# Kernel tuning notes

Measured on AMD Instinct MI355X. Metric: run time of the kernel, lower is better.

The kernel has to match this reference:

```python
import jax, jax.numpy as jnp
import numpy as np

P_EPS = 1e-6            # nn.PairwiseDistance default eps
ALPHA = 0.25
STD_TARGET = 1.0
NUM_COMMUNITIES = 512   # C = number of unique community ids
BIG = 1e30              # masking value for hard-negative min


def setup_inputs() -> dict:
    key = jax.random.key(0)
    k1, k2, k3 = jax.random.split(key, 3)
    B, N, D, C = 1, 100000, 128, NUM_COMMUNITIES
    node_features = jax.random.normal(k1, (B, N, D), dtype=jnp.float32)
    # row 0: a permutation of node indices; row 1: community of that node.
    perm = jax.random.permutation(k2, N).astype(jnp.int32)
    comm_per_node = jnp.concatenate([
        jnp.arange(C, dtype=jnp.int32),  # guarantee every community appears
        jax.random.randint(k3, (N - C,), 0, C, dtype=jnp.int32),
    ])
    community_belong_list = jnp.stack([perm, comm_per_node[perm]])  # [2, N]
    return {"node_features": node_features, "community_belong_list": community_belong_list}


def reference(node_features, community_belong_list):
    B, N, D = node_features.shape
    C = NUM_COMMUNITIES
    dt = node_features.dtype

    # ---- _community_inverse_permute: invert row-0 permutation, reorder columns ----
    perm = community_belong_list[0]
    inv = jnp.zeros((N,), perm.dtype).at[perm].add(jnp.arange(N, dtype=perm.dtype))
    cbl = community_belong_list[:, inv]          # row0 == arange(N) after this
    comm = cbl[1]                                # [N] community id per node
    src = node_features[:, cbl[0], :]            # [B,N,D] gather (identity order)

    # ---- groupby sum / count -> community means ----
    comm_sum = jnp.zeros((B, C, D), dt).at[:, comm, :].add(src)        # [B,C,D]
    counts = jnp.zeros((C,), dt).at[comm].add(jnp.asarray(1.0, dt))   # [C]
    comm_mean = comm_sum / counts[None, :, None]                      # [B,C,D]

    # ---- cdist(node_features, comm_mean, p=2) -> [B,N,C] ----
    x2 = jnp.sum(node_features * node_features, -1)                   # [B,N]
    c2 = jnp.sum(comm_mean * comm_mean, -1)                           # [B,C]
    dots = jnp.einsum('bnd,bcd->bnc', node_features, comm_mean)
    distance = jnp.sqrt(jnp.maximum(x2[:, :, None] + c2[:, None, :] - 2.0 * dots, 0.0))

    # ---- leave-one-out community mean per node, positive distance ----
    cnt_pn = counts[comm]                                             # [N]
    cnt_m1 = jnp.maximum(cnt_pn - 1.0, 1.0)                           # [N]
    x_minus = jnp.where((cnt_pn == 1.0)[None, :, None], jnp.asarray(0.0, dt), src)
    loo_mean = (comm_sum[:, comm, :] - x_minus) / cnt_m1[None, :, None]
    pos_dist = jnp.sqrt(jnp.sum((loo_mean - src + P_EPS) ** 2, -1))   # [B,N]

    # ---- negatives: all communities except the node's own ----
    own = distance[:, jnp.arange(N), comm]                            # [B,N]
    mean_neg = (jnp.sum(distance, -1) - own) / (C - 1)                # [B,N]
    pos_mask = jnp.zeros((N, C), bool).at[jnp.arange(N), comm].set(True)
    hard_neg = jnp.min(jnp.where(pos_mask[None], jnp.asarray(BIG, dt), distance), -1)

    trip_mean = jnp.maximum(pos_dist - mean_neg + ALPHA, 0.0)
    trip_min = jnp.maximum(pos_dist - hard_neg + ALPHA, 0.0)

    # ---- groupby std (unbiased) per community per feature ----
    sq = jnp.zeros((B, C, D), dt).at[:, comm, :].add((src - comm_mean[:, comm, :]) ** 2)
    std = jnp.sqrt(sq / jnp.maximum(counts - 1.0, 1.0)[None, :, None])

    return (trip_mean.mean(), trip_min.mean(), ((std - STD_TARGET) ** 2).mean())
```

## Files before the change

### kernel.cpp

```cpp
#include <hip/hip_runtime.h>

#define NCOMM 512
#define DIM   128
#define ALPHA 0.25f
#define PEPS  1e-6f
#define BIGF  1e30f
#define TILE_C 16
#define NT    (NCOMM / TILE_C)

typedef __attribute__((ext_vector_type(8))) _Float16 f16x8;
typedef __attribute__((ext_vector_type(4))) float f32x4;

#define GLOAD_LDS16(g, l) __builtin_amdgcn_global_load_lds( \
    (const __attribute__((address_space(1))) void*)(g), \
    (__attribute__((address_space(3))) void*)(l), 16, 0, 0)


__global__ void k_prep(const int* __restrict__ cbl, int* __restrict__ comm,
                       int* __restrict__ counts, int N) {
    __shared__ int h[NCOMM];
    int t = threadIdx.x;
    h[t] = 0; h[t + 256] = 0;
    __syncthreads();
    int i = blockIdx.x * 256 + t;
    if (i < N) {
        int p = cbl[i];
        int c = cbl[N + i];
        comm[p] = c;
        atomicAdd(&h[c], 1);
    }
    __syncthreads();
    int v = h[t];        if (v) atomicAdd(&counts[t], v);
    v = h[t + 256];      if (v) atomicAdd(&counts[t + 256], v);
}

__global__ void k_scan(const int* __restrict__ counts, int* __restrict__ offsets,
                       int* __restrict__ cursor, float* __restrict__ countf) {
    __shared__ int sc[NCOMM];
    int t = threadIdx.x;
    int v0 = counts[t];
    sc[t] = v0;
    __syncthreads();
    for (int off = 1; off < NCOMM; off <<= 1) {
        int v = (t >= off) ? sc[t - off] : 0;
        __syncthreads();
        sc[t] += v;
        __syncthreads();
    }
    int excl = sc[t] - v0;
    offsets[t] = excl;
    cursor[t]  = excl;
    countf[t]  = (float)v0;
}

__global__ void k_sort(const int* __restrict__ comm, int* __restrict__ cursor,
                       int* __restrict__ sorted, int N) {
    __shared__ int h[NCOMM], hb[NCOMM];
    int t = threadIdx.x;
    h[t] = 0; h[t + 256] = 0;
    __syncthreads();
    int j0 = blockIdx.x * 1024 + t;
    int cs[4];
    #pragma unroll
    for (int q = 0; q < 4; ++q) {
        int j = j0 + q * 256;
        cs[q] = (j < N) ? comm[j] : -1;
        if (cs[q] >= 0) atomicAdd(&h[cs[q]], 1);
    }
    __syncthreads();
    int v = h[t];        if (v) hb[t] = atomicAdd(&cursor[t], v);
    v = h[t + 256];      if (v) hb[t + 256] = atomicAdd(&cursor[t + 256], v);
    __syncthreads();
    #pragma unroll
    for (int q = 0; q < 4; ++q) {
        int j = j0 + q * 256;
        if (cs[q] >= 0) {
            int p = atomicAdd(&hb[cs[q]], 1);
            sorted[p] = j;
        }
    }
}


__global__ void __launch_bounds__(256) k_stats(
        const float* __restrict__ NF,
        const int* __restrict__ sorted, const int* __restrict__ offsets,
        const int* __restrict__ counts,
        float* __restrict__ comm_sum,
        _Float16* __restrict__ CMh, _Float16* __restrict__ CMl,
        float* __restrict__ c2, float* __restrict__ accum) {
    __shared__ int ridx[512];
    __shared__ float4 bufS[256], bufQ[256];
    int c = blockIdx.x, t = threadIdx.x;
    int d4 = t & 31, r = t >> 5;
    int cnt = counts[c], base = offsets[c];
    const float4* NF4 = (const float4*)NF;

    float4 s4 = make_float4(0.f, 0.f, 0.f, 0.f);
    float4 q4 = make_float4(0.f, 0.f, 0.f, 0.f);
    for (int chunk = 0; chunk < cnt; chunk += 512) {
        int m = min(cnt - chunk, 512);
        for (int i = t; i < m; i += 256) ridx[i] = sorted[base + chunk + i];
        __syncthreads();
        for (int i = r; i < m; i += 8) {
            float4 v = NF4[(size_t)ridx[i] * 32 + d4];
            s4.x += v.x; s4.y += v.y; s4.z += v.z; s4.w += v.w;
            q4.x = fmaf(v.x, v.x, q4.x); q4.y = fmaf(v.y, v.y, q4.y);
            q4.z = fmaf(v.z, v.z, q4.z); q4.w = fmaf(v.w, v.w, q4.w);
        }
        __syncthreads();
    }
    bufS[t] = s4; bufQ[t] = q4;
    __syncthreads();
    if (t < 128) {
        float4 a = bufS[t], b = bufS[t + 128];
        a.x += b.x; a.y += b.y; a.z += b.z; a.w += b.w; bufS[t] = a;
        float4 e = bufQ[t], f = bufQ[t + 128];
        e.x += f.x; e.y += f.y; e.z += f.z; e.w += f.w; bufQ[t] = e;
    }
    __syncthreads();
    if (t < 64) {
        float4 a = bufS[t], b = bufS[t + 64];
        a.x += b.x; a.y += b.y; a.z += b.z; a.w += b.w; bufS[t] = a;
        float4 e = bufQ[t], f = bufQ[t + 64];
        e.x += f.x; e.y += f.y; e.z += f.z; e.w += f.w; bufQ[t] = e;
    }
    __syncthreads();
    if (t < 32) {
        float4 a = bufS[t], b = bufS[t + 32];
        a.x += b.x; a.y += b.y; a.z += b.z; a.w += b.w;
        float4 e = bufQ[t], f = bufQ[t + 32];
        e.x += f.x; e.y += f.y; e.z += f.z; e.w += f.w;
        float sarr[4] = {a.x, a.y, a.z, a.w};
        float qarr[4] = {e.x, e.y, e.z, e.w};
        float cf = (float)cnt;
        float mm = 0.f, ee = 0.f;
        #pragma unroll
        for (int k = 0; k < 4; ++k) {
            int d = t * 4 + k;
            float s = sarr[k];
            comm_sum[c * DIM + d] = s;
            float m = (cnt > 0) ? s / cf : 0.f;
            _Float16 mh = (_Float16)m;
            CMh[c * DIM + d] = mh;
            CMl[c * DIM + d] = (_Float16)(m - (float)mh);
            float varn = fmaxf(fmaf(-cf * m, m, qarr[k]), 0.f);
            float stdv = sqrtf(varn / fmaxf(cf - 1.f, 1.f));
            float er = stdv - 1.f;
            mm = fmaf(m, m, mm);
            ee = fmaf(er, er, ee);
        }
        #pragma unroll
        for (int msk = 1; msk < 32; msk <<= 1) {
            mm += __shfl_xor(mm, msk);
            ee += __shfl_xor(ee, msk);
        }
        if (t == 0) {
            c2[c] = mm;
            atomicAdd(&accum[2], ee);
        }
    }
}


__global__ void __launch_bounds__(256, 4) k_main(
        const float* __restrict__ NF,
        const _Float16* __restrict__ CMh,
        const _Float16* __restrict__ CMl,
        const float* __restrict__ comm_sum,
        const float* __restrict__ c2g,
        const float* __restrict__ countf,
        const int* __restrict__ comm,
        float* __restrict__ accum, int N) {
    __shared__ _Float16 Bst[4][2][2][TILE_C * 64];
    __shared__ float c2s[NCOMM];
    __shared__ int   comms[128];
    __shared__ float x2sh[128];
    __shared__ float sums[128], mins[128];
    __shared__ float red[8];

    int tid = threadIdx.x;
    int w  = tid >> 6;
    int l  = tid & 63;
    int lr = l & 15;
    int lk = l >> 4;
    int n0 = blockIdx.x * 128;

    int off0 = ((l >> 3) << 7) + (((l & 7) ^ ((l >> 3) & 7)) << 3);
    auto stage = [&](int ss, int b) {
        size_t g0 = (size_t)(ss >> 1) * 2048 + (ss & 1) * 64 + off0;
        _Float16* lh = &Bst[w][b][0][0];
        _Float16* ll = &Bst[w][b][1][0];
        GLOAD_LDS16(CMh + g0,        lh);
        GLOAD_LDS16(CMh + g0 + 1024, lh + 512);
        GLOAD_LDS16(CMl + g0,        ll);
        GLOAD_LDS16(CMl + g0 + 1024, ll + 512);
    };
    stage(0, 0);

    c2s[tid]       = c2g[tid];
    c2s[tid + 256] = c2g[tid + 256];
    if (tid < 128) {
        int gn = n0 + tid;
        comms[tid] = (gn < N) ? comm[gn] : -1;
    }

    f16x8 ah[2][4];
    #pragma unroll
    for (int mf = 0; mf < 2; ++mf) {
        int n = n0 + w * 32 + mf * 16 + lr;
        const float4* src = (const float4*)NF + (size_t)n * 32 + lk * 2;
        float p2 = 0.f;
        #pragma unroll
        for (int ks = 0; ks < 4; ++ks) {
            float4 v0 = make_float4(0.f, 0.f, 0.f, 0.f), v1 = v0;
            if (n < N) { v0 = src[ks * 8]; v1 = src[ks * 8 + 1]; }
            float fr[8] = {v0.x, v0.y, v0.z, v0.w, v1.x, v1.y, v1.z, v1.w};
            f16x8 hh;
            #pragma unroll
            for (int t = 0; t < 8; ++t) {
                hh[t] = (_Float16)fr[t];
                p2 = fmaf(fr[t], fr[t], p2);
            }
            ah[mf][ks] = hh;
        }
        p2 += __shfl_xor(p2, 16);
        p2 += __shfl_xor(p2, 32);
        if (lk == 0) x2sh[w * 32 + mf * 16 + lr] = -0.5f * p2;
    }
    __syncthreads();

    f32x4 x2v[2];
    int cnv[2][4];
    float sumv[2][4], minv[2][4];
    #pragma unroll
    for (int mf = 0; mf < 2; ++mf) {
        x2v[mf] = *(const f32x4*)&x2sh[w * 32 + mf * 16 + lk * 4];
        #pragma unroll
        for (int j = 0; j < 4; ++j) {
            cnv[mf][j] = comms[w * 32 + mf * 16 + lk * 4 + j];
            sumv[mf][j] = 0.f; minv[mf][j] = BIGF;
        }
    }

    int buf = 0;
    for (int tt = 0; tt < NT; ++tt) {
        f32x4 acc0, acc1;
        {
            stage(2 * tt + 1, buf ^ 1);
            asm volatile("s_waitcnt vmcnt(4)" ::: "memory");
            __builtin_amdgcn_sched_barrier(0);
            const _Float16* bhp = &Bst[w][buf][0][0];
            const _Float16* blp = &Bst[w][buf][1][0];
            acc0 = x2v[0]; acc1 = x2v[1];
            #pragma unroll
            for (int ks2 = 0; ks2 < 2; ++ks2) {
                int ch = (ks2 * 4 + lk) ^ (lr & 7);
                f16x8 bh = *(const f16x8*)&bhp[(size_t)(lr * 64 + ch * 8)];
                f16x8 bl = *(const f16x8*)&blp[(size_t)(lr * 64 + ch * 8)];
                acc0 = __builtin_amdgcn_mfma_f32_16x16x32_f16(ah[0][ks2], bh, acc0, 0, 0, 0);
                acc1 = __builtin_amdgcn_mfma_f32_16x16x32_f16(ah[1][ks2], bh, acc1, 0, 0, 0);
                acc0 = __builtin_amdgcn_mfma_f32_16x16x32_f16(ah[0][ks2], bl, acc0, 0, 0, 0);
                acc1 = __builtin_amdgcn_mfma_f32_16x16x32_f16(ah[1][ks2], bl, acc1, 0, 0, 0);
            }
            buf ^= 1;
        }
        {
            if (tt + 1 < NT) {
                stage(2 * tt + 2, buf ^ 1);
                asm volatile("s_waitcnt vmcnt(4)" ::: "memory");
            } else {
                asm volatile("s_waitcnt vmcnt(0)" ::: "memory");
            }
            __builtin_amdgcn_sched_barrier(0);
            const _Float16* bhp = &Bst[w][buf][0][0];
            const _Float16* blp = &Bst[w][buf][1][0];
            #pragma unroll
            for (int ks2 = 0; ks2 < 2; ++ks2) {
                int ch = (ks2 * 4 + lk) ^ (lr & 7);
                f16x8 bh = *(const f16x8*)&bhp[(size_t)(lr * 64 + ch * 8)];
                f16x8 bl = *(const f16x8*)&blp[(size_t)(lr * 64 + ch * 8)];
                acc0 = __builtin_amdgcn_mfma_f32_16x16x32_f16(ah[0][2 + ks2], bh, acc0, 0, 0, 0);
                acc1 = __builtin_amdgcn_mfma_f32_16x16x32_f16(ah[1][2 + ks2], bh, acc1, 0, 0, 0);
                acc0 = __builtin_amdgcn_mfma_f32_16x16x32_f16(ah[0][2 + ks2], bl, acc0, 0, 0, 0);
                acc1 = __builtin_amdgcn_mfma_f32_16x16x32_f16(ah[1][2 + ks2], bl, acc1, 0, 0, 0);
            }
            int ccol = tt * TILE_C + lr;
            float c2v = c2s[ccol];
            #pragma unroll
            for (int j = 0; j < 4; ++j) {
                float d2a = fmaf(-2.f, acc0[j], c2v);
                float da  = __builtin_amdgcn_sqrtf(fmaxf(d2a, 0.f));
                sumv[0][j] += da;
                minv[0][j] = fminf(minv[0][j], (cnv[0][j] == ccol) ? BIGF : da);
                float d2b = fmaf(-2.f, acc1[j], c2v);
                float db  = __builtin_amdgcn_sqrtf(fmaxf(d2b, 0.f));
                sumv[1][j] += db;
                minv[1][j] = fminf(minv[1][j], (cnv[1][j] == ccol) ? BIGF : db);
            }
            buf ^= 1;
        }
    }

    #pragma unroll
    for (int mf = 0; mf < 2; ++mf)
        #pragma unroll
        for (int j = 0; j < 4; ++j) {
            float sv = sumv[mf][j], mv = minv[mf][j];
            #pragma unroll
            for (int msk = 1; msk < 16; msk <<= 1) {
                sv += __shfl_xor(sv, msk);
                mv = fminf(mv, __shfl_xor(mv, msk));
            }
            if (lr == 0) {
                int idx = w * 32 + mf * 16 + lk * 4 + j;
                sums[idx] = sv; mins[idx] = mv;
            }
        }
    __syncthreads();

    float tmean = 0.f, tminv = 0.f;
    {
        int ln = tid >> 1, half = tid & 1;
        int n = n0 + ln;
        if (n < N) {
            int cnode = comms[ln];
            float cf  = countf[cnode];
            float cm1 = fmaxf(cf - 1.f, 1.f);
            float rs  = 1.f / cm1;
            bool single = (cf == 1.f);
            const float4* srow = (const float4*)NF + (size_t)n * 32 + half * 16;
            const float4* csum = (const float4*)(comm_sum + (size_t)cnode * DIM) + half * 16;
            float q = 0.f, dot = 0.f;
            #pragma unroll
            for (int m = 0; m < 16; ++m) {
                float4 sv = srow[m];
                float4 cs = csum[m];
                float4 xm = single ? make_float4(0.f, 0.f, 0.f, 0.f) : sv;
                float lx = (cs.x - xm.x) * rs - sv.x + PEPS;
                float ly = (cs.y - xm.y) * rs - sv.y + PEPS;
                float lz = (cs.z - xm.z) * rs - sv.z + PEPS;
                float lw = (cs.w - xm.w) * rs - sv.w + PEPS;
                q = fmaf(lx, lx, fmaf(ly, ly, fmaf(lz, lz, fmaf(lw, lw, q))));
                dot = fmaf(sv.x, cs.x, fmaf(sv.y, cs.y, fmaf(sv.z, cs.z, fmaf(sv.w, cs.w, dot))));
            }
            q   += __shfl_xor(q, 1);
            dot += __shfl_xor(dot, 1);
            if (half == 0) {
                float pos = sqrtf(q);
                float x2 = -2.f * x2sh[ln];
                float ownd2 = x2 + c2s[cnode] - 2.f * (dot / cf);
                float own = sqrtf(fmaxf(ownd2, 0.f));
                float mean_neg = (sums[ln] - own) * (1.f / (float)(NCOMM - 1));
                tmean = fmaxf(pos - mean_neg + ALPHA, 0.f);
                tminv = fmaxf(pos - mins[ln] + ALPHA, 0.f);
            }
        }
    }
    #pragma unroll
    for (int msk = 1; msk < 64; msk <<= 1) {
        tmean += __shfl_xor(tmean, msk);
        tminv += __shfl_xor(tminv, msk);
    }
    if ((tid & 63) == 0) { red[w * 2] = tmean; red[w * 2 + 1] = tminv; }
    __syncthreads();
    if (tid == 0) {
        atomicAdd(&accum[0], red[0] + red[2] + red[4] + red[6]);
        atomicAdd(&accum[1], red[1] + red[3] + red[5] + red[7]);
    }
}

__global__ void k_final(const float* __restrict__ accum, float* __restrict__ out, int N) {
    if (threadIdx.x == 0) {
        out[0] = accum[0] / (float)N;
        out[1] = accum[1] / (float)N;
        out[2] = accum[2] / (float)(NCOMM * DIM);
    }
}


extern "C" void kernel_launch(void* const* d_in, const int* in_sizes, int n_in,
                              void* d_out, int out_size, void* d_ws, size_t ws_size,
                              hipStream_t stream) {
    const float* NF  = (const float*)d_in[0];
    const int*   CBL = (const int*)d_in[1];
    int N = in_sizes[1] / 2;
    if (N <= 0) return;

    char* ws = (char*)d_ws;
    float* accum   = (float*)ws;
    int*   counts  = (int*)(ws + 16);
    int*   cursor  = (int*)(ws + 16 + 2048);
    int*   offsets = (int*)(ws + 16 + 2 * 2048);
    float* countf  = (float*)(ws + 16 + 3 * 2048);
    float* c2      = (float*)(ws + 16 + 4 * 2048);
    char* p = ws + 16 + 5 * 2048;
    int* comm   = (int*)p; p += (size_t)N * 4;
    int* sorted = (int*)p; p += (size_t)N * 4;
    float* comm_sum = (float*)p; p += (size_t)NCOMM * DIM * 4;
    _Float16* CMh = (_Float16*)p; p += (size_t)NCOMM * DIM * 2;
    _Float16* CMl = (_Float16*)p;

    hipMemsetAsync(d_ws, 0, 16 + 2048, stream);

    int nb = (N + 255) / 256;
    k_prep<<<nb, 256, 0, stream>>>(CBL, comm, counts, N);
    k_scan<<<1, NCOMM, 0, stream>>>(counts, offsets, cursor, countf);
    int nb4 = (N + 1023) / 1024;
    k_sort<<<nb4, 256, 0, stream>>>(comm, cursor, sorted, N);
    k_stats<<<NCOMM, 256, 0, stream>>>(NF, sorted, offsets, counts,
                                       comm_sum, CMh, CMl, c2, accum);
    int mb = (N + 127) / 128;
    k_main<<<mb, 256, 0, stream>>>(NF, CMh, CMl, comm_sum, c2, countf,
                                   comm, accum, N);
    k_final<<<1, 64, 0, stream>>>(accum, (float*)d_out, N);
}
```

Baseline: 127.9 us.

## Drop fp16 low-part correction of community means and deepen LDS pipeline

The hi/lo fp16 split of the community means is removed, so the distance GEMM uses a single fp16 B operand, which halves the MFMA count and the B-tile traffic. The LDS staging goes from double to four-deep buffering with adjusted vmcnt waits, and the gather loop in the stats kernel is unrolled by four to keep more loads in flight. The cost is lower precision in the dot products: the means are now rounded to fp16 with no correction term, and this error feeds into the distances and the hard-negative min.

```diff
diff --git a/kernel.cpp b/kernel.cpp
--- a/kernel.cpp
+++ b/kernel.cpp
@@ -87,7 +87,7 @@
         const int* __restrict__ sorted, const int* __restrict__ offsets,
         const int* __restrict__ counts,
         float* __restrict__ comm_sum,
-        _Float16* __restrict__ CMh, _Float16* __restrict__ CMl,
+        _Float16* __restrict__ CMh,
         float* __restrict__ c2, float* __restrict__ accum) {
     __shared__ int ridx[512];
     __shared__ float4 bufS[256], bufQ[256];
@@ -102,7 +102,27 @@
         int m = min(cnt - chunk, 512);
         for (int i = t; i < m; i += 256) ridx[i] = sorted[base + chunk + i];
         __syncthreads();
-        for (int i = r; i < m; i += 8) {
+        int i = r;
+        for (; i + 24 < m; i += 32) {
+            int a0 = ridx[i], a1 = ridx[i + 8], a2 = ridx[i + 16], a3 = ridx[i + 24];
+            float4 v0 = NF4[(size_t)a0 * 32 + d4];
+            float4 v1 = NF4[(size_t)a1 * 32 + d4];
+            float4 v2 = NF4[(size_t)a2 * 32 + d4];
+            float4 v3 = NF4[(size_t)a3 * 32 + d4];
+            s4.x += v0.x; s4.y += v0.y; s4.z += v0.z; s4.w += v0.w;
+            q4.x = fmaf(v0.x, v0.x, q4.x); q4.y = fmaf(v0.y, v0.y, q4.y);
+            q4.z = fmaf(v0.z, v0.z, q4.z); q4.w = fmaf(v0.w, v0.w, q4.w);
+            s4.x += v1.x; s4.y += v1.y; s4.z += v1.z; s4.w += v1.w;
+            q4.x = fmaf(v1.x, v1.x, q4.x); q4.y = fmaf(v1.y, v1.y, q4.y);
+            q4.z = fmaf(v1.z, v1.z, q4.z); q4.w = fmaf(v1.w, v1.w, q4.w);
+            s4.x += v2.x; s4.y += v2.y; s4.z += v2.z; s4.w += v2.w;
+            q4.x = fmaf(v2.x, v2.x, q4.x); q4.y = fmaf(v2.y, v2.y, q4.y);
+            q4.z = fmaf(v2.z, v2.z, q4.z); q4.w = fmaf(v2.w, v2.w, q4.w);
+            s4.x += v3.x; s4.y += v3.y; s4.z += v3.z; s4.w += v3.w;
+            q4.x = fmaf(v3.x, v3.x, q4.x); q4.y = fmaf(v3.y, v3.y, q4.y);
+            q4.z = fmaf(v3.z, v3.z, q4.z); q4.w = fmaf(v3.w, v3.w, q4.w);
+        }
+        for (; i < m; i += 8) {
             float4 v = NF4[(size_t)ridx[i] * 32 + d4];
             s4.x += v.x; s4.y += v.y; s4.z += v.z; s4.w += v.w;
             q4.x = fmaf(v.x, v.x, q4.x); q4.y = fmaf(v.y, v.y, q4.y);
@@ -141,9 +161,7 @@
             float s = sarr[k];
             comm_sum[c * DIM + d] = s;
             float m = (cnt > 0) ? s / cf : 0.f;
-            _Float16 mh = (_Float16)m;
-            CMh[c * DIM + d] = mh;
-            CMl[c * DIM + d] = (_Float16)(m - (float)mh);
+            CMh[c * DIM + d] = (_Float16)m;
             float varn = fmaxf(fmaf(-cf * m, m, qarr[k]), 0.f);
             float stdv = sqrtf(varn / fmaxf(cf - 1.f, 1.f));
             float er = stdv - 1.f;
@@ -166,13 +184,12 @@
 __global__ void __launch_bounds__(256, 4) k_main(
         const float* __restrict__ NF,
         const _Float16* __restrict__ CMh,
-        const _Float16* __restrict__ CMl,
         const float* __restrict__ comm_sum,
         const float* __restrict__ c2g,
         const float* __restrict__ countf,
         const int* __restrict__ comm,
         float* __restrict__ accum, int N) {
-    __shared__ _Float16 Bst[4][2][2][TILE_C * 64];
+    __shared__ _Float16 Bst[4][4][TILE_C * 64];
     __shared__ float c2s[NCOMM];
     __shared__ int   comms[128];
     __shared__ float x2sh[128];
@@ -187,16 +204,14 @@
     int n0 = blockIdx.x * 128;
 
     int off0 = ((l >> 3) << 7) + (((l & 7) ^ ((l >> 3) & 7)) << 3);
+    const _Float16* gsrc = CMh + off0;
     auto stage = [&](int ss, int b) {
-        size_t g0 = (size_t)(ss >> 1) * 2048 + (ss & 1) * 64 + off0;
-        _Float16* lh = &Bst[w][b][0][0];
-        _Float16* ll = &Bst[w][b][1][0];
-        GLOAD_LDS16(CMh + g0,        lh);
-        GLOAD_LDS16(CMh + g0 + 1024, lh + 512);
-        GLOAD_LDS16(CMl + g0,        ll);
-        GLOAD_LDS16(CMl + g0 + 1024, ll + 512);
+        const _Float16* g = gsrc + (size_t)(ss >> 1) * 2048 + (ss & 1) * 64;
+        _Float16* lh = &Bst[w][b][0];
+        GLOAD_LDS16(g,        lh);
+        GLOAD_LDS16(g + 1024, lh + 512);
     };
-    stage(0, 0);
+    stage(0, 0); stage(1, 1); stage(2, 2);
 
     c2s[tid]       = c2g[tid];
     c2s[tid + 256] = c2g[tid + 256];
@@ -243,47 +258,38 @@
         }
     }
 
-    int buf = 0;
     for (int tt = 0; tt < NT; ++tt) {
         f32x4 acc0, acc1;
         {
-            stage(2 * tt + 1, buf ^ 1);
-            asm volatile("s_waitcnt vmcnt(4)" ::: "memory");
+            int ssn = 2 * tt + 3;
+            if (ssn < 64) stage(ssn, ssn & 3);
+            if (tt <= 30) { asm volatile("s_waitcnt vmcnt(6)" ::: "memory"); }
+            else          { asm volatile("s_waitcnt vmcnt(2)" ::: "memory"); }
             __builtin_amdgcn_sched_barrier(0);
-            const _Float16* bhp = &Bst[w][buf][0][0];
-            const _Float16* blp = &Bst[w][buf][1][0];
+            const _Float16* bp = &Bst[w][(2 * tt) & 3][0];
             acc0 = x2v[0]; acc1 = x2v[1];
             #pragma unroll
             for (int ks2 = 0; ks2 < 2; ++ks2) {
                 int ch = (ks2 * 4 + lk) ^ (lr & 7);
-                f16x8 bh = *(const f16x8*)&bhp[(size_t)(lr * 64 + ch * 8)];
-                f16x8 bl = *(const f16x8*)&blp[(size_t)(lr * 64 + ch * 8)];
-                acc0 = __builtin_amdgcn_mfma_f32_16x16x32_f16(ah[0][ks2], bh, acc0, 0, 0, 0);
-                acc1 = __builtin_amdgcn_mfma_f32_16x16x32_f16(ah[1][ks2], bh, acc1, 0, 0, 0);
-                acc0 = __builtin_amdgcn_mfma_f32_16x16x32_f16(ah[0][ks2], bl, acc0, 0, 0, 0);
-                acc1 = __builtin_amdgcn_mfma_f32_16x16x32_f16(ah[1][ks2], bl, acc1, 0, 0, 0);
-            }
-            buf ^= 1;
+                f16x8 b = *(const f16x8*)&bp[(size_t)(lr * 64 + ch * 8)];
+                acc0 = __builtin_amdgcn_mfma_f32_16x16x32_f16(ah[0][ks2], b, acc0, 0, 0, 0);
+                acc1 = __builtin_amdgcn_mfma_f32_16x16x32_f16(ah[1][ks2], b, acc1, 0, 0, 0);
+            }
         }
         {
-            if (tt + 1 < NT) {
-                stage(2 * tt + 2, buf ^ 1);
-                asm volatile("s_waitcnt vmcnt(4)" ::: "memory");
-            } else {
-                asm volatile("s_waitcnt vmcnt(0)" ::: "memory");
-            }
+            int ssn = 2 * tt + 4;
+            if (ssn < 64) stage(ssn, ssn & 3);
+            if (tt <= 29)      { asm volatile("s_waitcnt vmcnt(6)" ::: "memory"); }
+            else if (tt == 30) { asm volatile("s_waitcnt vmcnt(4)" ::: "memory"); }
+            else               { asm volatile("s_waitcnt vmcnt(0)" ::: "memory"); }
             __builtin_amdgcn_sched_barrier(0);
-            const _Float16* bhp = &Bst[w][buf][0][0];
-            const _Float16* blp = &Bst[w][buf][1][0];
+            const _Float16* bp = &Bst[w][(2 * tt + 1) & 3][0];
             #pragma unroll
             for (int ks2 = 0; ks2 < 2; ++ks2) {
                 int ch = (ks2 * 4 + lk) ^ (lr & 7);
-                f16x8 bh = *(const f16x8*)&bhp[(size_t)(lr * 64 + ch * 8)];
-                f16x8 bl = *(const f16x8*)&blp[(size_t)(lr * 64 + ch * 8)];
-                acc0 = __builtin_amdgcn_mfma_f32_16x16x32_f16(ah[0][2 + ks2], bh, acc0, 0, 0, 0);
-                acc1 = __builtin_amdgcn_mfma_f32_16x16x32_f16(ah[1][2 + ks2], bh, acc1, 0, 0, 0);
-                acc0 = __builtin_amdgcn_mfma_f32_16x16x32_f16(ah[0][2 + ks2], bl, acc0, 0, 0, 0);
-                acc1 = __builtin_amdgcn_mfma_f32_16x16x32_f16(ah[1][2 + ks2], bl, acc1, 0, 0, 0);
+                f16x8 b = *(const f16x8*)&bp[(size_t)(lr * 64 + ch * 8)];
+                acc0 = __builtin_amdgcn_mfma_f32_16x16x32_f16(ah[0][2 + ks2], b, acc0, 0, 0, 0);
+                acc1 = __builtin_amdgcn_mfma_f32_16x16x32_f16(ah[1][2 + ks2], b, acc1, 0, 0, 0);
             }
             int ccol = tt * TILE_C + lr;
             float c2v = c2s[ccol];
@@ -298,7 +304,6 @@
                 sumv[1][j] += db;
                 minv[1][j] = fminf(minv[1][j], (cnv[1][j] == ccol) ? BIGF : db);
             }
-            buf ^= 1;
         }
     }
 
@@ -398,8 +403,7 @@
     int* comm   = (int*)p; p += (size_t)N * 4;
     int* sorted = (int*)p; p += (size_t)N * 4;
     float* comm_sum = (float*)p; p += (size_t)NCOMM * DIM * 4;
-    _Float16* CMh = (_Float16*)p; p += (size_t)NCOMM * DIM * 2;
-    _Float16* CMl = (_Float16*)p;
+    _Float16* CMh = (_Float16*)p;
 
     hipMemsetAsync(d_ws, 0, 16 + 2048, stream);
 
@@ -409,9 +413,9 @@
     int nb4 = (N + 1023) / 1024;
     k_sort<<<nb4, 256, 0, stream>>>(comm, cursor, sorted, N);
     k_stats<<<NCOMM, 256, 0, stream>>>(NF, sorted, offsets, counts,
-                                       comm_sum, CMh, CMl, c2, accum);
+                                       comm_sum, CMh, c2, accum);
     int mb = (N + 127) / 128;
-    k_main<<<mb, 256, 0, stream>>>(NF, CMh, CMl, comm_sum, c2, countf,
+    k_main<<<mb, 256, 0, stream>>>(NF, CMh, comm_sum, c2, countf,
                                    comm, accum, N);
     k_final<<<1, 64, 0, stream>>>(accum, (float*)d_out, N);
 }
```

New measurement: 119.6 us, median of 2. 6.5% less time.
